# Kernel tuning notes

Hardware: AMD Instinct MI355X
Metric: run time of the kernel (lower is better)

## Reference

```python
import jax, jax.numpy as jnp
import numpy as np

N_NODES = 20000
N_EDGES = 160000
F_IN = 256
N_CLASSES = 32
HEADS = 8
GAT_C = 128


def setup_inputs() -> dict:
    key = jax.random.key(0)
    ks = jax.random.split(key, 20)

    def w(k, shape, fan_in):
        return jax.random.normal(k, shape, dtype=jnp.float32) * (1.0 / np.sqrt(fan_in))

    return {
        "x": jax.random.normal(ks[0], (N_NODES, F_IN), dtype=jnp.float32),
        "edge_index": jax.random.randint(ks[1], (2, N_EDGES), 0, N_NODES, dtype=jnp.int64),
        # SAGEConv(256 -> 64): lin_l (bias) on aggregated neighbors, lin_r (no bias) on root
        "W_l1": w(ks[2], (F_IN, 64), F_IN), "b_l1": jnp.zeros((64,), jnp.float32),
        "W_r1": w(ks[3], (F_IN, 64), F_IN),
        # SAGEConv(64 -> 128)
        "W_l2": w(ks[4], (64, 128), 64), "b_l2": jnp.zeros((128,), jnp.float32),
        "W_r2": w(ks[5], (64, 128), 64),
        # GATConv(128 -> 128, heads=8, concat)
        "W_g": w(ks[6], (128, HEADS * GAT_C), 128),
        "att_src": w(ks[7], (HEADS, GAT_C), GAT_C),
        "att_dst": w(ks[8], (HEADS, GAT_C), GAT_C),
        "b_g": jnp.zeros((HEADS * GAT_C,), jnp.float32),
        # GCNConv(1024 -> 64), GCNConv(64 -> 32)
        "W_c1": w(ks[9], (HEADS * GAT_C, 64), HEADS * GAT_C), "b_c1": jnp.zeros((64,), jnp.float32),
        "W_c2": w(ks[10], (64, N_CLASSES), 64), "b_c2": jnp.zeros((N_CLASSES,), jnp.float32),
        # residual Linear(256 -> 64)
        "W_res": w(ks[11], (F_IN, 64), F_IN), "b_res": jnp.zeros((64,), jnp.float32),
    }


def _forward(x, edge_index, W_l1, b_l1, W_r1, W_l2, b_l2, W_r2,
             W_g, att_src, att_dst, b_g, W_c1, b_c1, W_c2, b_c2, W_res, b_res):
    n = x.shape[0]
    src, dst = edge_index[0], edge_index[1]  # messages flow src -> dst

    def sage(h, Wl, bl, Wr):
        # mean aggregation of neighbor features, then lin_l(agg) + lin_r(root)
        s = jax.ops.segment_sum(h[src], dst, num_segments=n)
        cnt = jax.ops.segment_sum(jnp.ones_like(src, dtype=h.dtype), dst, num_segments=n)
        mean = s / jnp.maximum(cnt, 1.0)[:, None]
        return mean @ Wl + bl + h @ Wr

    res_x = x @ W_res + b_res
    h = jax.nn.relu(sage(x, W_l1, b_l1, W_r1)) + res_x      # [N, 64]
    h = jax.nn.relu(sage(h, W_l2, b_l2, W_r2))              # [N, 128]

    # ---- GATConv with self-loops (PyG default) ----
    loop = jnp.arange(n, dtype=src.dtype)
    srcf = jnp.concatenate([src, loop])
    dstf = jnp.concatenate([dst, loop])

    hg = (h @ W_g).reshape(n, HEADS, GAT_C)                 # [N, H, C]
    a_s = jnp.sum(hg * att_src, axis=-1)                    # [N, H]
    a_d = jnp.sum(hg * att_dst, axis=-1)                    # [N, H]
    e = jax.nn.leaky_relu(a_s[srcf] + a_d[dstf], negative_slope=0.2)  # [Ef, H]
    m = jax.ops.segment_max(e, dstf, num_segments=n)
    e = jnp.exp(e - m[dstf])
    denom = jax.ops.segment_sum(e, dstf, num_segments=n)
    alpha = e / denom[dstf]                                 # softmax over incoming edges
    gat = jax.ops.segment_sum(alpha[:, :, None] * hg[srcf], dstf, num_segments=n)
    h = jax.nn.relu(gat.reshape(n, HEADS * GAT_C) + b_g)    # [N, 1024]

    # ---- GCNConv with self-loops and symmetric normalization ----
    deg = jax.ops.segment_sum(jnp.ones_like(srcf, dtype=h.dtype), dstf, num_segments=n)
    dinv = jax.lax.rsqrt(jnp.maximum(deg, 1.0))             # deg >= 1 via self-loops
    norm = (dinv[srcf] * dinv[dstf])[:, None]

    def gcn(h, W, b):
        hw = h @ W
        return jax.ops.segment_sum(norm * hw[srcf], dstf, num_segments=n) + b

    h = gcn(h, W_c1, b_c1)
    h = gcn(h, W_c2, b_c2)
    return jax.nn.log_softmax(h, axis=1)


def reference(x, edge_index, W_l1, b_l1, W_r1, W_l2, b_l2, W_r2,
              W_g, att_src, att_dst, b_g, W_c1, b_c1, W_c2, b_c2, W_res, b_res):
    return _forward(x, edge_index, W_l1, b_l1, W_r1, W_l2, b_l2, W_r2,
                    W_g, att_src, att_dst, b_g, W_c1, b_c1, W_c2, b_c2, W_res, b_res)
```

## Files before the change

### kernel.cpp

```cpp
#include <hip/hip_runtime.h>

#define NN 20000
#define NE 160000
#define NEF 180000
#define NB1 ((NN + 255) / 256)

typedef long long ll;
typedef __attribute__((ext_vector_type(4))) float f32x4;
typedef __attribute__((ext_vector_type(8))) short s16x8;

static __device__ __forceinline__ float b2f(ushort u) {
  return __uint_as_float(((unsigned)u) << 16);
}
static __device__ __forceinline__ ushort f2b(float f) {
  unsigned u = __float_as_uint(f);
  return (ushort)((u + 0x7fffu + ((u >> 16) & 1u)) >> 16);
}

template<int MF, int NF, int K, bool F32OUT>
__global__ __launch_bounds__(256) void gemm_mfma(
    const ushort* __restrict__ A, const ushort* __restrict__ Bt,
    const float* __restrict__ bias, void* __restrict__ Cv,
    int M, int N, int lda)
{
  const int wid  = threadIdx.x >> 6;
  const int lane = threadIdx.x & 63;
  const int wr = wid >> 1, wc = wid & 1;
  const int bm = blockIdx.y * (32 * MF) + wr * (16 * MF);
  const int bn = blockIdx.x * (32 * NF) + wc * (16 * NF);
  const int lr = lane & 15;
  const int ko = (lane >> 4) * 8;

  const ushort* pa[MF];
  const ushort* pb[NF];
  #pragma unroll
  for (int i = 0; i < MF; i++) {
    int r = min(bm + i * 16 + lr, M - 1);
    pa[i] = A + (ll)r * lda + ko;
  }
  #pragma unroll
  for (int j = 0; j < NF; j++) {
    int c = min(bn + j * 16 + lr, N - 1);
    pb[j] = Bt + (ll)c * K + ko;
  }

  f32x4 acc[MF][NF];
  #pragma unroll
  for (int i = 0; i < MF; i++)
    #pragma unroll
    for (int j = 0; j < NF; j++) acc[i][j] = {0.f, 0.f, 0.f, 0.f};

  #pragma unroll
  for (int k = 0; k < K; k += 32) {
    s16x8 af[MF], bf[NF];
    #pragma unroll
    for (int i = 0; i < MF; i++) af[i] = *(const s16x8*)(pa[i] + k);
    #pragma unroll
    for (int j = 0; j < NF; j++) bf[j] = *(const s16x8*)(pb[j] + k);
    #pragma unroll
    for (int i = 0; i < MF; i++)
      #pragma unroll
      for (int j = 0; j < NF; j++)
        acc[i][j] = __builtin_amdgcn_mfma_f32_16x16x32_bf16(af[i], bf[j], acc[i][j], 0, 0, 0);
  }

  const int rq = (lane >> 4) * 4;
  #pragma unroll
  for (int i = 0; i < MF; i++) {
    #pragma unroll
    for (int j = 0; j < NF; j++) {
      int col = bn + j * 16 + lr;
      if (col >= N) continue;
      float bv = bias ? bias[col] : 0.f;
      int rbase = bm + i * 16 + rq;
      #pragma unroll
      for (int r = 0; r < 4; r++) {
        int row = rbase + r;
        if (row >= M) continue;
        float v = acc[i][j][r] + bv;
        if (F32OUT) ((float*)Cv)[(ll)row * N + col] = v;
        else        ((ushort*)Cv)[(ll)row * N + col] = f2b(v);
      }
    }
  }
}

__global__ __launch_bounds__(256) void k_gat_apply_gcn1(
    const ushort* __restrict__ agg,
    const ushort* __restrict__ BtG,
    const ushort* __restrict__ Btc1,
    const float* __restrict__ b_g,
    ushort* __restrict__ hw64)
{
  __shared__ ushort gt[2][32][72];
  const int wc   = threadIdx.x >> 6;
  const int lane = threadIdx.x & 63;
  const int bm = blockIdx.x * 32;
  const int lr = lane & 15;
  const int ko = (lane >> 4) * 8;
  const int rq = (lane >> 4) * 4;

  const ushort* pa0 = agg + (ll)min(bm + lr,      NN - 1) * 1024 + ko;
  const ushort* pa1 = agg + (ll)min(bm + 16 + lr, NN - 1) * 1024 + ko;

  f32x4 o0 = {0.f, 0.f, 0.f, 0.f}, o1 = o0;

  #pragma unroll 2
  for (int ct = 0; ct < 16; ct++) {
    const int koff = (ct >> 1) * 128;
    const int cg = ct * 64 + wc * 16 + lr;
    const ushort* pb = BtG + (ll)cg * 128 + ko;
    f32x4 g0 = {0.f, 0.f, 0.f, 0.f}, g1 = g0;
    #pragma unroll
    for (int k = 0; k < 128; k += 32) {
      s16x8 a0 = *(const s16x8*)(pa0 + koff + k);
      s16x8 a1 = *(const s16x8*)(pa1 + koff + k);
      s16x8 bb = *(const s16x8*)(pb + k);
      g0 = __builtin_amdgcn_mfma_f32_16x16x32_bf16(a0, bb, g0, 0, 0, 0);
      g1 = __builtin_amdgcn_mfma_f32_16x16x32_bf16(a1, bb, g1, 0, 0, 0);
    }
    float bv = b_g[cg];
    #pragma unroll
    for (int r = 0; r < 4; r++) {
      gt[ct & 1][rq + r][wc * 16 + lr]      = f2b(fmaxf(g0[r] + bv, 0.f));
      gt[ct & 1][16 + rq + r][wc * 16 + lr] = f2b(fmaxf(g1[r] + bv, 0.f));
    }
    __syncthreads();
    const ushort* qb = Btc1 + (ll)(wc * 16 + lr) * 1024 + ct * 64 + ko;
    #pragma unroll
    for (int k = 0; k < 64; k += 32) {
      s16x8 a0 = *(const s16x8*)&gt[ct & 1][lr][k + ko];
      s16x8 a1 = *(const s16x8*)&gt[ct & 1][16 + lr][k + ko];
      s16x8 bb = *(const s16x8*)(qb + k);
      o0 = __builtin_amdgcn_mfma_f32_16x16x32_bf16(a0, bb, o0, 0, 0, 0);
      o1 = __builtin_amdgcn_mfma_f32_16x16x32_bf16(a1, bb, o1, 0, 0, 0);
    }
  }
  int col = wc * 16 + lr;
  #pragma unroll
  for (int r = 0; r < 4; r++) {
    int row0 = bm + rq + r, row1 = bm + 16 + rq + r;
    if (row0 < NN) hw64[(ll)row0 * 64 + col] = f2b(o0[r]);
    if (row1 < NN) hw64[(ll)row1 * 64 + col] = f2b(o1[r]);
  }
}

struct PrepEnt { const float* W; ushort* Bt; int N; int K; int base; };
struct Prep { PrepEnt e[8]; int total; };

__global__ void k_setup(const float* __restrict__ x, ushort* __restrict__ xb, Prep p,
                        const float* __restrict__ b_res, const float* __restrict__ b_l1,
                        const float* __restrict__ b_l2, float* __restrict__ bias192,
                        float* __restrict__ bias256,
                        const float* __restrict__ W_g, const float* __restrict__ att_s,
                        const float* __restrict__ att_d, ushort* __restrict__ watt_t) {
  ll t = (ll)blockIdx.x * 256 + threadIdx.x;
  const ll T0 = (ll)NN * 64;
  if (t < T0) {
    ll i = t * 4;
    float4 v = *(const float4*)(x + i);
    ushort4 o;
    o.x = f2b(v.x); o.y = f2b(v.y); o.z = f2b(v.z); o.w = f2b(v.w);
    *(ushort4*)(xb + i) = o;
    return;
  }
  t -= T0;
  if (t < p.total) {
    int tt = (int)t;
    #pragma unroll
    for (int i = 0; i < 8; i++) {
      int sz = p.e[i].N * p.e[i].K;
      if (tt >= p.e[i].base && tt < p.e[i].base + sz) {
        int loc = tt - p.e[i].base;
        int n = loc / p.e[i].K, k = loc - n * p.e[i].K;
        p.e[i].Bt[loc] = f2b(p.e[i].W[(ll)k * p.e[i].N + n]);
      }
    }
    return;
  }
  t -= p.total;
  if (t < 256) {
    int tt = (int)t;
    if (tt < 64) bias192[tt] = b_res[tt];
    else if (tt < 128) bias192[tt] = 0.f;
    else if (tt < 192) bias192[tt] = b_l1[tt - 128];
    bias256[tt] = (tt < 128) ? 0.f : b_l2[tt - 128];
    return;
  }
  t -= 256;
  if (t < 2048) {
    int k = (int)t >> 4;
    int col = (int)t & 15;
    int h = col & 7;
    const float* av = (col < 8) ? (att_s + h * 128) : (att_d + h * 128);
    const float* wrow = W_g + (ll)k * 1024 + h * 128;
    float s = 0.f;
    for (int j = 0; j < 128; j++) s += wrow[j] * av[j];
    watt_t[col * 128 + k] = f2b(s);
  }
}

__global__ void k_counti(const int* __restrict__ dst, int* __restrict__ icnt) {
  int e = blockIdx.x * 256 + threadIdx.x;
  if (e < NE) atomicAdd(&icnt[dst[e]], 1);
}

__global__ __launch_bounds__(256) void k_scan1(const int* __restrict__ icnt,
                                               int* __restrict__ rowptr,
                                               int* __restrict__ bsum) {
  __shared__ int sd[256];
  int t = threadIdx.x;
  int i = blockIdx.x * 256 + t;
  int v = (i < NN) ? icnt[i] + 1 : 0;
  sd[t] = v;
  __syncthreads();
  #pragma unroll
  for (int o = 1; o < 256; o <<= 1) {
    int u = (t >= o) ? sd[t - o] : 0;
    __syncthreads();
    sd[t] += u;
    __syncthreads();
  }
  if (i < NN) rowptr[i] = sd[t] - v;
  if (t == 255) bsum[blockIdx.x] = sd[255];
}

__global__ __launch_bounds__(128) void k_scan2(const int* __restrict__ bsum,
                                               int* __restrict__ boff) {
  __shared__ int sd[128];
  int t = threadIdx.x;
  int v = (t < NB1) ? bsum[t] : 0;
  sd[t] = v;
  __syncthreads();
  #pragma unroll
  for (int o = 1; o < 128; o <<= 1) {
    int u = (t >= o) ? sd[t - o] : 0;
    __syncthreads();
    sd[t] += u;
    __syncthreads();
  }
  if (t < NB1) boff[t] = sd[t] - v;
}

__global__ void k_scan3(int* __restrict__ rowptr, const int* __restrict__ boff,
                        int* __restrict__ cur, const int* __restrict__ icnt,
                        float* __restrict__ dinv) {
  int i = blockIdx.x * 256 + threadIdx.x;
  if (i >= NN) return;
  int r = rowptr[i] + boff[i >> 8];
  rowptr[i] = r;
  cur[i] = r;
  dinv[i] = rsqrtf((float)icnt[i] + 1.0f);
  if (i == 0) rowptr[NN] = NEF;
}

__global__ void k_scatter(const int* __restrict__ dst, int* __restrict__ cur,
                          int* __restrict__ eid) {
  int t = blockIdx.x * 256 + threadIdx.x;
  if (t >= NEF) return;
  int d = (t < NE) ? dst[t] : t - NE;
  int p = atomicAdd(&cur[d], 1);
  eid[p] = t;
}

template<int C, int STRIDE, bool ADD_RES>
__global__ __launch_bounds__(256) void k_sage_csr(
    const int* __restrict__ rowptr, const int* __restrict__ eid,
    const int* __restrict__ src, const ushort* __restrict__ feat,
    const ushort* __restrict__ linr, const ushort* __restrict__ resx,
    ushort* __restrict__ out)
{
  int node = blockIdx.x * 4 + (threadIdx.x >> 6);
  int lane = threadIdx.x & 63;
  if (node >= NN) return;
  int b = rowptr[node], e = rowptr[node + 1];
  float a0 = 0.f, a1 = 0.f;
  int n = 0;
  for (int base = b; base < e; base += 64) {
    int m = min(64, e - base);
    int sreg = -1;
    if (lane < m) {
      int ed = eid[base + lane];
      sreg = (ed < NE) ? src[ed] : -1;
    }
    for (int i = 0; i < m; i++) {
      int s = __shfl(sreg, i);
      if (s >= 0) {
        a0 += b2f(feat[(ll)s * STRIDE + lane]);
        if (C == 128) a1 += b2f(feat[(ll)s * STRIDE + lane + 64]);
        n++;
      }
    }
  }
  float inv = 1.f / fmaxf((float)n, 1.f);
  {
    float v = a0 * inv + b2f(linr[(ll)node * STRIDE + lane]);
    v = fmaxf(v, 0.f);
    if (ADD_RES) v += b2f(resx[(ll)node * STRIDE + lane]);
    out[(ll)node * C + lane] = f2b(v);
  }
  if (C == 128) {
    float v = a1 * inv + b2f(linr[(ll)node * STRIDE + lane + 64]);
    v = fmaxf(v, 0.f);
    out[(ll)node * C + lane + 64] = f2b(v);
  }
}

__global__ void k_gat_softmax(const int* __restrict__ rowptr, const int* __restrict__ eid,
                              const int* __restrict__ src, const float* __restrict__ asd,
                              float* __restrict__ alpha, float* __restrict__ invden) {
  int t = blockIdx.x * 256 + threadIdx.x;
  if (t >= NN * 8) return;
  int node = t >> 3, h = t & 7;
  int b = rowptr[node], e = rowptr[node + 1];
  float ad = asd[(ll)node * 16 + 8 + h];
  float mx = -3.0e38f;
  for (int p = b; p < e; p++) {
    int ed = eid[p];
    int s = (ed < NE) ? src[ed] : node;
    float v = asd[(ll)s * 16 + h] + ad;
    v = (v > 0.f) ? v : 0.2f * v;
    mx = fmaxf(mx, v);
  }
  float sum = 0.f;
  for (int p = b; p < e; p++) {
    int ed = eid[p];
    int s = (ed < NE) ? src[ed] : node;
    float v = asd[(ll)s * 16 + h] + ad;
    v = (v > 0.f) ? v : 0.2f * v;
    float ex = expf(v - mx);
    alpha[(ll)p * 8 + h] = ex;
    sum += ex;
  }
  invden[t] = 1.f / sum;
}

__global__ __launch_bounds__(128) void k_gat_agg(
    const int* __restrict__ rowptr, const int* __restrict__ eid,
    const int* __restrict__ src, const float* __restrict__ alpha,
    const float* __restrict__ invden, const ushort* __restrict__ h2b,
    ushort* __restrict__ agg)
{
  __shared__ int s_l[64];
  __shared__ float al[64 * 8];
  __shared__ float inv_s[8];
  int node = blockIdx.x;
  int c = threadIdx.x;
  int b = rowptr[node], e = rowptr[node + 1];
  if (c < 8) inv_s[c] = invden[node * 8 + c];
  float acc[8] = {0.f, 0.f, 0.f, 0.f, 0.f, 0.f, 0.f, 0.f};
  for (int c0 = b; c0 < e; c0 += 64) {
    int m = min(64, e - c0);
    if (c < m) { int ed = eid[c0 + c]; s_l[c] = (ed < NE) ? src[ed] : node; }
    for (int idx = c; idx < m * 8; idx += 128) al[idx] = alpha[(ll)c0 * 8 + idx];
    __syncthreads();
    for (int i = 0; i < m; i++) {
      float v = b2f(h2b[(ll)s_l[i] * 128 + c]);
      float4 aa = *(const float4*)&al[i * 8];
      float4 ab = *(const float4*)&al[i * 8 + 4];
      acc[0] = fmaf(aa.x, v, acc[0]);
      acc[1] = fmaf(aa.y, v, acc[1]);
      acc[2] = fmaf(aa.z, v, acc[2]);
      acc[3] = fmaf(aa.w, v, acc[3]);
      acc[4] = fmaf(ab.x, v, acc[4]);
      acc[5] = fmaf(ab.y, v, acc[5]);
      acc[6] = fmaf(ab.z, v, acc[6]);
      acc[7] = fmaf(ab.w, v, acc[7]);
    }
    __syncthreads();
  }
  #pragma unroll
  for (int h = 0; h < 8; h++)
    agg[(ll)node * 1024 + h * 128 + c] = f2b(acc[h] * inv_s[h]);
}

template<int C, bool FUSE_LSM>
__global__ __launch_bounds__(256) void k_gcn_csr(
    const int* __restrict__ rowptr, const int* __restrict__ eid,
    const int* __restrict__ src, const float* __restrict__ dinv,
    const ushort* __restrict__ hw, const float* __restrict__ bias,
    void* __restrict__ outv)
{
  const int npb = 256 / C;
  int node = blockIdx.x * npb + threadIdx.x / C;
  int c = threadIdx.x & (C - 1);
  if (node >= NN) return;
  int b = rowptr[node], e = rowptr[node + 1];
  float acc = 0.f;
  for (int base = b; base < e; base += C) {
    int m = min(C, e - base);
    int sreg = 0;
    float dreg = 0.f;
    if (c < m) {
      int ed = eid[base + c];
      sreg = (ed < NE) ? src[ed] : node;
      dreg = dinv[sreg];
    }
    for (int i = 0; i < m; i++) {
      int s  = __shfl(sreg, i, C);
      float dv = __shfl(dreg, i, C);
      acc = fmaf(dv, b2f(hw[(ll)s * C + c]), acc);
    }
  }
  float v = acc * dinv[node] + bias[c];
  if (!FUSE_LSM) {
    ((ushort*)outv)[(ll)node * C + c] = f2b(v);
  } else {
    float mx = v;
    #pragma unroll
    for (int o = 16; o > 0; o >>= 1) mx = fmaxf(mx, __shfl_xor(mx, o, 32));
    float s = expf(v - mx);
    #pragma unroll
    for (int o = 16; o > 0; o >>= 1) s += __shfl_xor(s, o, 32);
    ((float*)outv)[(ll)node * C + c] = v - mx - logf(s);
  }
}

extern "C" void kernel_launch(void* const* d_in, const int* in_sizes, int n_in,
                              void* d_out, int out_size, void* d_ws, size_t ws_size,
                              hipStream_t stream) {
  const float* x     = (const float*)d_in[0];
  const int*   ei    = (const int*)d_in[1];
  const float* W_l1  = (const float*)d_in[2];
  const float* b_l1  = (const float*)d_in[3];
  const float* W_r1  = (const float*)d_in[4];
  const float* W_l2  = (const float*)d_in[5];
  const float* b_l2  = (const float*)d_in[6];
  const float* W_r2  = (const float*)d_in[7];
  const float* W_g   = (const float*)d_in[8];
  const float* att_s = (const float*)d_in[9];
  const float* att_d = (const float*)d_in[10];
  const float* b_g   = (const float*)d_in[11];
  const float* W_c1  = (const float*)d_in[12];
  const float* b_c1  = (const float*)d_in[13];
  const float* W_c2  = (const float*)d_in[14];
  const float* b_c2  = (const float*)d_in[15];
  const float* W_res = (const float*)d_in[16];
  const float* b_res = (const float*)d_in[17];
  const int* src = ei;
  const int* dst = ei + NE;
  float* out = (float*)d_out;

  float* Wf = (float*)d_ws;
  size_t off = 0;
  auto take = [&](size_t n) { float* p = Wf + off; off += (n + 3) & ~(size_t)3; return p; };
  ushort* xb    = (ushort*)take((size_t)NN * 128);
  ushort* C192  = (ushort*)take((size_t)NN * 96);
  ushort* h1    = (ushort*)take((size_t)NN * 32);
  ushort* C256  = (ushort*)take((size_t)NN * 128);
  ushort* h2    = (ushort*)take((size_t)NN * 64);
  ushort* agg   = (ushort*)take((size_t)NN * 512);
  ushort* hw64  = (ushort*)take((size_t)NN * 32);
  ushort* acc64 = (ushort*)take((size_t)NN * 32);
  ushort* hw32  = (ushort*)take((size_t)NN * 16);
  ushort* Bt192 = (ushort*)take(192 * 256 / 2);
  ushort* Bt256 = (ushort*)take(256 * 64 / 2);
  ushort* BtG   = (ushort*)take(1024 * 128 / 2);
  ushort* Btc1  = (ushort*)take(64 * 1024 / 2);
  ushort* Btc2  = (ushort*)take(32 * 64 / 2);
  ushort* watt_t= (ushort*)take(16 * 128 / 2);
  float* bias192 = take(192);
  float* bias256 = take(256);
  int*   icnt   = (int*)take(NN);
  int*   rowptr = (int*)take(NN + 1);
  int*   cur    = (int*)take(NN);
  int*   eidb   = (int*)take(NEF);
  int*   bsum   = (int*)take(NB1);
  int*   boff   = (int*)take(NB1);
  float* dinv   = take(NN);
  float* asd    = take((size_t)NN * 16);
  float* alpha  = take((size_t)NEF * 8);
  float* invden = take((size_t)NN * 8);
  (void)ws_size; (void)in_sizes; (void)n_in; (void)out_size;

  auto nb = [](ll t) { return dim3((unsigned)((t + 255) / 256)); };

  hipMemsetAsync(icnt, 0, NN * sizeof(int), stream);
  k_counti<<<nb(NE), 256, 0, stream>>>(dst, icnt);
  k_scan1<<<NB1, 256, 0, stream>>>(icnt, rowptr, bsum);
  k_scan2<<<1, 128, 0, stream>>>(bsum, boff);
  k_scan3<<<nb(NN), 256, 0, stream>>>(rowptr, boff, cur, icnt, dinv);
  k_scatter<<<nb(NEF), 256, 0, stream>>>(dst, cur, eidb);

  Prep pp;
  int base = 0;
  auto ent = [&](int i, const float* W, ushort* Bt, int N_, int K_) {
    pp.e[i] = {W, Bt, N_, K_, base}; base += N_ * K_;
  };
  ent(0, W_res, Bt192,             64, 256);
  ent(1, W_l1,  Bt192 + 64 * 256,  64, 256);
  ent(2, W_r1,  Bt192 + 128 * 256, 64, 256);
  ent(3, W_l2,  Bt256,             128, 64);
  ent(4, W_r2,  Bt256 + 128 * 64,  128, 64);
  ent(5, W_g,   BtG,               1024, 128);
  ent(6, W_c1,  Btc1,              64, 1024);
  ent(7, W_c2,  Btc2,              32, 64);
  pp.total = base;
  k_setup<<<nb((ll)NN * 64 + base + 256 + 2048), 256, 0, stream>>>(
      x, xb, pp, b_res, b_l1, b_l2, bias192, bias256, W_g, att_s, att_d, watt_t);

  gemm_mfma<2, 2, 256, false><<<dim3(3, 313), 256, 0, stream>>>(
      xb, Bt192, bias192, C192, NN, 192, 256);
  k_sage_csr<64, 192, true><<<nb((ll)NN * 64), 256, 0, stream>>>(
      rowptr, eidb, src, C192 + 64, C192 + 128, C192, h1);

  gemm_mfma<2, 2, 64, false><<<dim3(4, 313), 256, 0, stream>>>(
      h1, Bt256, bias256, C256, NN, 256, 64);
  k_sage_csr<128, 256, false><<<nb((ll)NN * 64), 256, 0, stream>>>(
      rowptr, eidb, src, C256, C256 + 128, nullptr, h2);

  gemm_mfma<2, 1, 128, true><<<dim3(1, 313), 256, 0, stream>>>(
      h2, watt_t, nullptr, asd, NN, 16, 128);
  k_gat_softmax<<<nb((ll)NN * 8), 256, 0, stream>>>(
      rowptr, eidb, src, asd, alpha, invden);
  k_gat_agg<<<dim3(NN), 128, 0, stream>>>(
      rowptr, eidb, src, alpha, invden, h2, agg);
  k_gat_apply_gcn1<<<dim3(625), 256, 0, stream>>>(agg, BtG, Btc1, b_g, hw64);
  k_gcn_csr<64, false><<<nb((ll)NN * 64), 256, 0, stream>>>(
      rowptr, eidb, src, dinv, hw64, b_c1, acc64);

  gemm_mfma<2, 1, 64, false><<<dim3(1, 313), 256, 0, stream>>>(
      acc64, Btc2, nullptr, hw32, NN, 32, 64);
  k_gcn_csr<32, true><<<nb((ll)NN * 32), 256, 0, stream>>>(
      rowptr, eidb, src, dinv, hw32, b_c2, out);
}
```

Baseline: 260.2 us.

## Halve row tile in fused GAT-apply/GCN1 kernel to double block count

The fused GAT output projection plus GCN1 kernel now processes 16 rows per block instead of 32, and each loop step covers 128 GAT columns (two 64-column halves) instead of 64. This gives 1250 blocks instead of 625, for better occupancy across the CUs, and halves the number of __syncthreads barriers per block. In exchange, each BtG and Btc1 weight fragment is reused across only one 16-row MFMA tile, so total weight traffic from L2 doubles.

```diff
diff --git a/kernel.cpp b/kernel.cpp
--- a/kernel.cpp
+++ b/kernel.cpp
@@ -92,56 +92,54 @@
     const float* __restrict__ b_g,
     ushort* __restrict__ hw64)
 {
-  __shared__ ushort gt[2][32][72];
+  __shared__ ushort gt[2][2][16][72];
   const int wc   = threadIdx.x >> 6;
   const int lane = threadIdx.x & 63;
-  const int bm = blockIdx.x * 32;
+  const int bm = blockIdx.x * 16;
   const int lr = lane & 15;
   const int ko = (lane >> 4) * 8;
   const int rq = (lane >> 4) * 4;
 
-  const ushort* pa0 = agg + (ll)min(bm + lr,      NN - 1) * 1024 + ko;
-  const ushort* pa1 = agg + (ll)min(bm + 16 + lr, NN - 1) * 1024 + ko;
-
-  f32x4 o0 = {0.f, 0.f, 0.f, 0.f}, o1 = o0;
+  const ushort* pa0 = agg + (ll)min(bm + lr, NN - 1) * 1024 + ko;
+
+  f32x4 o0 = {0.f, 0.f, 0.f, 0.f};
 
   #pragma unroll 2
-  for (int ct = 0; ct < 16; ct++) {
-    const int koff = (ct >> 1) * 128;
-    const int cg = ct * 64 + wc * 16 + lr;
-    const ushort* pb = BtG + (ll)cg * 128 + ko;
-    f32x4 g0 = {0.f, 0.f, 0.f, 0.f}, g1 = g0;
+  for (int p = 0; p < 8; p++) {
+    const int koff = p * 128;
+    const int cg0 = p * 128 + wc * 16 + lr;
+    const int cg1 = cg0 + 64;
+    const ushort* pb0 = BtG + (ll)cg0 * 128 + ko;
+    const ushort* pb1 = BtG + (ll)cg1 * 128 + ko;
+    f32x4 gA = {0.f, 0.f, 0.f, 0.f}, gB = gA;
     #pragma unroll
     for (int k = 0; k < 128; k += 32) {
       s16x8 a0 = *(const s16x8*)(pa0 + koff + k);
-      s16x8 a1 = *(const s16x8*)(pa1 + koff + k);
-      s16x8 bb = *(const s16x8*)(pb + k);
-      g0 = __builtin_amdgcn_mfma_f32_16x16x32_bf16(a0, bb, g0, 0, 0, 0);
-      g1 = __builtin_amdgcn_mfma_f32_16x16x32_bf16(a1, bb, g1, 0, 0, 0);
-    }
-    float bv = b_g[cg];
+      gA = __builtin_amdgcn_mfma_f32_16x16x32_bf16(a0, *(const s16x8*)(pb0 + k), gA, 0, 0, 0);
+      gB = __builtin_amdgcn_mfma_f32_16x16x32_bf16(a0, *(const s16x8*)(pb1 + k), gB, 0, 0, 0);
+    }
+    float bv0 = b_g[cg0], bv1 = b_g[cg1];
     #pragma unroll
     for (int r = 0; r < 4; r++) {
-      gt[ct & 1][rq + r][wc * 16 + lr]      = f2b(fmaxf(g0[r] + bv, 0.f));
-      gt[ct & 1][16 + rq + r][wc * 16 + lr] = f2b(fmaxf(g1[r] + bv, 0.f));
-    }
-    __syncthreads();
-    const ushort* qb = Btc1 + (ll)(wc * 16 + lr) * 1024 + ct * 64 + ko;
-    #pragma unroll
-    for (int k = 0; k < 64; k += 32) {
-      s16x8 a0 = *(const s16x8*)&gt[ct & 1][lr][k + ko];
-      s16x8 a1 = *(const s16x8*)&gt[ct & 1][16 + lr][k + ko];
-      s16x8 bb = *(const s16x8*)(qb + k);
-      o0 = __builtin_amdgcn_mfma_f32_16x16x32_bf16(a0, bb, o0, 0, 0, 0);
-      o1 = __builtin_amdgcn_mfma_f32_16x16x32_bf16(a1, bb, o1, 0, 0, 0);
-    }
+      gt[p & 1][0][rq + r][wc * 16 + lr] = f2b(fmaxf(gA[r] + bv0, 0.f));
+      gt[p & 1][1][rq + r][wc * 16 + lr] = f2b(fmaxf(gB[r] + bv1, 0.f));
+    }
+    __syncthreads();
+    const ushort* qb = Btc1 + (ll)(wc * 16 + lr) * 1024 + p * 128 + ko;
+    o0 = __builtin_amdgcn_mfma_f32_16x16x32_bf16(
+        *(const s16x8*)&gt[p & 1][0][lr][ko],      *(const s16x8*)(qb),      o0, 0, 0, 0);
+    o0 = __builtin_amdgcn_mfma_f32_16x16x32_bf16(
+        *(const s16x8*)&gt[p & 1][0][lr][32 + ko], *(const s16x8*)(qb + 32), o0, 0, 0, 0);
+    o0 = __builtin_amdgcn_mfma_f32_16x16x32_bf16(
+        *(const s16x8*)&gt[p & 1][1][lr][ko],      *(const s16x8*)(qb + 64), o0, 0, 0, 0);
+    o0 = __builtin_amdgcn_mfma_f32_16x16x32_bf16(
+        *(const s16x8*)&gt[p & 1][1][lr][32 + ko], *(const s16x8*)(qb + 96), o0, 0, 0, 0);
   }
   int col = wc * 16 + lr;
   #pragma unroll
   for (int r = 0; r < 4; r++) {
-    int row0 = bm + rq + r, row1 = bm + 16 + rq + r;
-    if (row0 < NN) hw64[(ll)row0 * 64 + col] = f2b(o0[r]);
-    if (row1 < NN) hw64[(ll)row1 * 64 + col] = f2b(o1[r]);
+    int row = bm + rq + r;
+    if (row < NN) hw64[(ll)row * 64 + col] = f2b(o0[r]);
   }
 }
 
@@ -515,7 +513,7 @@
       rowptr, eidb, src, asd, alpha, invden);
   k_gat_agg<<<dim3(NN), 128, 0, stream>>>(
       rowptr, eidb, src, alpha, invden, h2, agg);
-  k_gat_apply_gcn1<<<dim3(625), 256, 0, stream>>>(agg, BtG, Btc1, b_g, hw64);
+  k_gat_apply_gcn1<<<dim3(1250), 256, 0, stream>>>(agg, BtG, Btc1, b_g, hw64);
   k_gcn_csr<64, false><<<nb((ll)NN * 64), 256, 0, stream>>>(
       rowptr, eidb, src, dinv, hw64, b_c1, acc64);
 
```

Result: slower. 274.1 us (+5.3%).
